# Optimization experiments

Measured on AMD Instinct MI355X. Metric: run time of the kernel, lower is better.

Reference implementation:

```python
import jax, jax.numpy as jnp
import numpy as np

STRIDE, PAD, DIL, DG, K = 1, 1, 1, 1, 3


def _conv2d(x, w, b, stride, pad):
    out = jax.lax.conv_general_dilated(
        x, w, (stride, stride), [(pad, pad), (pad, pad)],
        dimension_numbers=("NCHW", "OIHW", "NCHW"))
    return out + b[None, :, None, None]


def _deform_conv(x, weight, bias, offset, mask):
    # x: [B,C,H,W]; offset: [B, 2*DG*K*K, Ho, Wo] (y,x interleaved per tap);
    # mask: [B, DG*K*K, Ho, Wo]; weight: [Cout, C, K, K]
    B, C, H, W = x.shape
    Cout = weight.shape[0]
    KK = K * K
    Ho, Wo = offset.shape[2], offset.shape[3]
    Cg = C // DG

    off = offset.reshape(B, DG, KK, 2, Ho, Wo)
    dy, dx = off[:, :, :, 0], off[:, :, :, 1]          # [B,DG,KK,Ho,Wo]

    ky = (jnp.arange(KK) // K).astype(jnp.float32) * DIL
    kx = (jnp.arange(KK) % K).astype(jnp.float32) * DIL
    oy = (jnp.arange(Ho).astype(jnp.float32) * STRIDE - PAD)
    ox = (jnp.arange(Wo).astype(jnp.float32) * STRIDE - PAD)
    py = dy + ky[None, None, :, None, None] + oy[None, None, None, :, None]
    px = dx + kx[None, None, :, None, None] + ox[None, None, None, None, :]

    y0 = jnp.floor(py)
    x0 = jnp.floor(px)
    wy = py - y0
    wx = px - x0
    y0i = y0.astype(jnp.int32)
    x0i = x0.astype(jnp.int32)

    x_g = x.reshape(B, DG, Cg, H * W)
    val = jnp.zeros((B, DG, Cg, KK, Ho, Wo), dtype=x.dtype)
    corners = [(y0i, x0i, (1 - wy) * (1 - wx)),
               (y0i, x0i + 1, (1 - wy) * wx),
               (y0i + 1, x0i, wy * (1 - wx)),
               (y0i + 1, x0i + 1, wy * wx)]
    for iy, ix, wgt in corners:
        valid = ((iy >= 0) & (iy < H) & (ix >= 0) & (ix < W)).astype(x.dtype)
        idx = jnp.clip(iy, 0, H - 1) * W + jnp.clip(ix, 0, W - 1)  # [B,DG,KK,Ho,Wo]
        g = jnp.take_along_axis(x_g, idx.reshape(B, DG, 1, KK * Ho * Wo), axis=3)
        g = g.reshape(B, DG, Cg, KK, Ho, Wo)
        val = val + g * (wgt * valid)[:, :, None]

    m = mask.reshape(B, DG, 1, KK, Ho, Wo)
    val = (val * m).reshape(B, C, KK, Ho, Wo)
    out = jnp.einsum("bckhw,ock->bohw", val, weight.reshape(Cout, C, KK))
    return out + bias[None, :, None, None]


def setup_inputs() -> dict:
    key = jax.random.key(0)
    ks = jax.random.split(key, 5)
    B, C, H, W, Cout = 8, 64, 128, 128, 64
    x = jax.random.normal(ks[0], (B, C, H, W), dtype=jnp.float32)
    stdv = 1.0 / np.sqrt(C * K * K)
    weight = jax.random.uniform(ks[1], (Cout, C, K, K), minval=-stdv, maxval=stdv, dtype=jnp.float32)
    bias = jnp.zeros((Cout,), dtype=jnp.float32)
    # conv_offset params are zero-init in the original; use small random values
    offset_w = jax.random.normal(ks[2], (3 * DG * K * K, C, K, K), dtype=jnp.float32) * 0.01
    offset_b = jax.random.normal(ks[3], (3 * DG * K * K,), dtype=jnp.float32) * 0.01
    return {"x": x, "weight": weight, "bias": bias, "offset_w": offset_w, "offset_b": offset_b}


def reference(x, weight, bias, offset_w, offset_b):
    split = 2 * DG * K * K
    out = _conv2d(x, offset_w, offset_b, STRIDE, PAD)
    offset = out[:, :split]
    mask = jax.nn.sigmoid(out[:, split:])
    return _deform_conv(x, weight, bias, offset, mask)
```

## Files before the change

### kernel.cpp

```cpp
#include <hip/hip_runtime.h>
#include <hip/hip_bf16.h>
#include <math.h>

#define HH 128
#define WW 128
#define HW 16384
#define BATCH 8

#define TR 8
#define TC 16
#define HALO 2
#define PR 12
#define PC 20
#define NPX (PR * PC)
#define PST 34

typedef __attribute__((ext_vector_type(8))) _Float16 f16x8;
typedef __attribute__((ext_vector_type(2))) _Float16 f16x2;
typedef __attribute__((ext_vector_type(16))) float f32x16;
typedef __attribute__((ext_vector_type(4))) unsigned int u32x4;

union FragU { f16x8 v; unsigned int u[4]; u32x4 q; f16x2 h[4]; };

static __device__ __forceinline__ unsigned short f2h(float f) {
    _Float16 h = (_Float16)f;
    return *(unsigned short*)&h;
}
static __device__ __forceinline__ float h2f(unsigned short u) {
    _Float16 h = *(_Float16*)&u;
    return (float)h;
}

static __device__ __forceinline__ f16x8 bilerp_frag(
    u32x4 r00, u32x4 r01, u32x4 r10, u32x4 r11,
    f16x2 W0, f16x2 W1, f16x2 W2, f16x2 W3)
{
    FragU a, b, c, d, bf;
    a.q = r00; b.q = r01; c.q = r10; d.q = r11;
#pragma unroll
    for (int i = 0; i < 4; ++i) {
        f16x2 s = a.h[i] * W0;
        s = __builtin_elementwise_fma(b.h[i], W1, s);
        s = __builtin_elementwise_fma(c.h[i], W2, s);
        s = __builtin_elementwise_fma(d.h[i], W3, s);
        bf.h[i] = s;
    }
    return bf.v;
}

#define PADDR(PX, C) ((PX) * PST + ((C) << 2))

__global__ __launch_bounds__(256) void prep_kernel(
    const float* __restrict__ weight,
    const float* __restrict__ offset_w,
    unsigned short* __restrict__ wA,
    unsigned short* __restrict__ owA)
{
    int id = blockIdx.x * 256 + threadIdx.x;
    if (id < 4608) {
        int m = id / 2304;
        int rem = id % 2304;
        int kk = rem >> 8;
        int s = (rem >> 6) & 3;
        int l = id & 63;
        int cout = m * 32 + (l & 31);
        int cbase = s * 16 + 8 * (l >> 5);
#pragma unroll
        for (int j = 0; j < 8; ++j) {
            wA[id * 8 + j] = f2h(weight[(cout * 64 + cbase + j) * 9 + kk]);
        }
        return;
    }
    int id2 = id - 4608;
    if (id2 < 2304) {
        int kk = id2 >> 8;
        int s = (id2 >> 6) & 3;
        int l = id2 & 63;
        int cout = l & 31;
        int cbase = s * 16 + 8 * (l >> 5);
#pragma unroll
        for (int j = 0; j < 8; ++j) {
            float v = (cout < 27) ? offset_w[(cout * 64 + cbase + j) * 9 + kk] : 0.0f;
            owA[id2 * 8 + j] = f2h(v);
        }
    }
}

__global__ __launch_bounds__(256) void transform_kernel(
    const float* __restrict__ x,
    unsigned int* __restrict__ xT)
{
    __shared__ unsigned int lds[64][33];
    int bid = blockIdx.x;
    int b = bid & 7;
    int pix0 = (bid >> 3) << 6;
    int t = threadIdx.x;
    int px = t & 63;
    int cp0 = (t >> 6) * 8;

    const float* xb = x + (size_t)b * 64 * HW + pix0 + px;
#pragma unroll
    for (int it = 0; it < 8; ++it) {
        int cpair = cp0 + it;
        float lo = xb[(size_t)(2 * cpair) * HW];
        float hi = xb[(size_t)(2 * cpair + 1) * HW];
        lds[px][cpair] = ((unsigned int)f2h(hi) << 16) | f2h(lo);
    }
    __syncthreads();

    int wpx = t >> 2, qq = t & 3;
    unsigned int* dst = xT + ((size_t)b * HW + pix0 + wpx) * 32 + qq * 8;
    u32x4 a, c;
#pragma unroll
    for (int j = 0; j < 4; ++j) a[j] = lds[wpx][qq * 8 + j];
#pragma unroll
    for (int j = 0; j < 4; ++j) c[j] = lds[wpx][qq * 8 + 4 + j];
    *(u32x4*)dst = a;
    *(u32x4*)(dst + 4) = c;
}

__global__ __launch_bounds__(256, 4) void fused_kernel(
    const unsigned int* __restrict__ xT,
    const unsigned short* __restrict__ wA,
    const unsigned short* __restrict__ owA,
    const float* __restrict__ bias,
    const float* __restrict__ offset_b,
    float* __restrict__ out)
{
    __shared__ unsigned int patch[NPX * PST];
    __shared__ unsigned short red[4][27][32];

    int t = threadIdx.x;
    int lane = t & 63;
    int wid = t >> 6;
    int bid = blockIdx.x;
    int b = bid & 7;
    int tile = bid >> 3;
    int ho0 = (tile >> 3) * TR;
    int wo0 = (tile & 7) * TC;
    int py0 = ho0 - HALO;
    int px0 = wo0 - HALO;

    int q = lane & 31;
    int hi = lane >> 5;
    int ho = ho0 + 2 * wid + (q >> 4);
    int wo = wo0 + (q & 15);
    int p = ho * WW + wo;

    const unsigned int* xb = xT + (size_t)b * HW * 32;
    const f16x8* wAv = (const f16x8*)wA;
    const f16x8* owAv = (const f16x8*)owA;

#pragma unroll
    for (int it = 0; it < 8; ++it) {
        int id = it * 256 + t;
        if (id < NPX * 8) {
            int px = id >> 3;
            int c = id & 7;
            int row = px / PC;
            int col = px - row * PC;
            int iy = py0 + row;
            int ix = px0 + col;
            bool okpx = ((unsigned)iy < 128u) && ((unsigned)ix < 128u);
            int yc = min(max(iy, 0), HH - 1);
            int xc = min(max(ix, 0), WW - 1);
            u32x4 v = *(const u32x4*)(xb + (size_t)(yc * WW + xc) * 32 + c * 4);
#pragma unroll
            for (int j = 0; j < 4; ++j) v[j] = okpx ? v[j] : 0u;
            *(u32x4*)&patch[PADDR(px, c)] = v;
        }
    }
    __syncthreads();

    {
        f32x16 acc1 = {};
#pragma unroll
        for (int kk = 0; kk < 9; ++kk) {
            int jy = ho + kk / 3 - 1 - py0;
            int jx = wo + kk % 3 - 1 - px0;
            int ptap = jy * PC + jx;
#pragma unroll
            for (int s = 0; s < 4; ++s) {
                FragU bf;
                bf.q = *(const u32x4*)&patch[PADDR(ptap, 2 * s + hi)];
                acc1 = __builtin_amdgcn_mfma_f32_32x32x16_f16(
                    owAv[(kk * 4 + s) * 64 + lane], bf.v, acc1, 0, 0, 0);
            }
        }
#pragma unroll
        for (int r = 0; r < 16; ++r) {
            int cout = (r & 3) + 8 * (r >> 2) + 4 * hi;
            if (cout < 27) {
                float a = acc1[r] + offset_b[cout];
                if (cout >= 18) a = 1.0f / (1.0f + __expf(-a));
                red[wid][cout][q] = f2h(a);
            }
        }
    }

    f32x16 acc[2];
#pragma unroll
    for (int m = 0; m < 2; ++m) {
#pragma unroll
        for (int r = 0; r < 16; ++r) {
            acc[m][r] = bias[m * 32 + (r & 3) + 8 * (r >> 2) + 4 * hi];
        }
    }

    for (int kk = 0; kk < 9; ++kk) {
        float dy = h2f(red[wid][2 * kk][q]);
        float dx = h2f(red[wid][2 * kk + 1][q]);
        float mm = h2f(red[wid][18 + kk][q]);

        float py = dy + (float)(kk / 3 + ho - 1);
        float px = dx + (float)(kk % 3 + wo - 1);
        float y0f = floorf(py), x0f = floorf(px);
        float wy = py - y0f, wx = px - x0f;
        int y0 = (int)y0f, x0 = (int)x0f;
        int y1 = y0 + 1, x1 = x0 + 1;
        bool y0ok = (unsigned)y0 < 128u, y1ok = (unsigned)y1 < 128u;
        bool x0ok = (unsigned)x0 < 128u, x1ok = (unsigned)x1 < 128u;
        float w0 = (y0ok && x0ok) ? (1.0f - wy) * (1.0f - wx) * mm : 0.0f;
        float w1 = (y0ok && x1ok) ? (1.0f - wy) * wx * mm : 0.0f;
        float w2 = (y1ok && x0ok) ? wy * (1.0f - wx) * mm : 0.0f;
        float w3 = (y1ok && x1ok) ? wy * wx * mm : 0.0f;
        int y0c = min(max(y0, 0), 127), y1c = min(max(y1, 0), 127);
        int x0c = min(max(x0, 0), 127), x1c = min(max(x1, 0), 127);

        f16x2 W0 = {(_Float16)w0, (_Float16)w0};
        f16x2 W1 = {(_Float16)w1, (_Float16)w1};
        f16x2 W2 = {(_Float16)w2, (_Float16)w2};
        f16x2 W3 = {(_Float16)w3, (_Float16)w3};

        int jy0 = y0c - py0, jy1 = y1c - py0;
        int jx0 = x0c - px0, jx1 = x1c - px0;
        bool inp = ((unsigned)jy0 < (unsigned)PR) && ((unsigned)jy1 < (unsigned)PR) &&
                   ((unsigned)jx0 < (unsigned)PC) && ((unsigned)jx1 < (unsigned)PC);

#define P2_STEP(S, R00, R01, R10, R11) {                                    \
            f16x8 A0 = wAv[(kk * 4 + (S)) * 64 + lane];                     \
            f16x8 A1 = wAv[(36 + kk * 4 + (S)) * 64 + lane];                \
            f16x8 bf = bilerp_frag(R00, R01, R10, R11, W0, W1, W2, W3);     \
            acc[0] = __builtin_amdgcn_mfma_f32_32x32x16_f16(A0, bf, acc[0], 0, 0, 0); \
            acc[1] = __builtin_amdgcn_mfma_f32_32x32x16_f16(A1, bf, acc[1], 0, 0, 0); \
        }

        if (__all(inp)) {
            int p00 = jy0 * PC + jx0;
            int p01 = jy0 * PC + jx1;
            int p10 = jy1 * PC + jx0;
            int p11 = jy1 * PC + jx1;
#define LRD(PX, S) (*(const u32x4*)&patch[PADDR(PX, 2 * (S) + hi)])
            P2_STEP(0, LRD(p00,0), LRD(p01,0), LRD(p10,0), LRD(p11,0));
            P2_STEP(1, LRD(p00,1), LRD(p01,1), LRD(p10,1), LRD(p11,1));
            P2_STEP(2, LRD(p00,2), LRD(p01,2), LRD(p10,2), LRD(p11,2));
            P2_STEP(3, LRD(p00,3), LRD(p01,3), LRD(p10,3), LRD(p11,3));
#undef LRD
        } else {
            int o00 = (y0c * WW + x0c) * 32 + (hi << 2);
            int o01 = (y0c * WW + x1c) * 32 + (hi << 2);
            int o10 = (y1c * WW + x0c) * 32 + (hi << 2);
            int o11 = (y1c * WW + x1c) * 32 + (hi << 2);
#define GRD(O, S) (*(const u32x4*)(xb + (O) + (S) * 8))
            P2_STEP(0, GRD(o00,0), GRD(o01,0), GRD(o10,0), GRD(o11,0));
            P2_STEP(1, GRD(o00,1), GRD(o01,1), GRD(o10,1), GRD(o11,1));
            P2_STEP(2, GRD(o00,2), GRD(o01,2), GRD(o10,2), GRD(o11,2));
            P2_STEP(3, GRD(o00,3), GRD(o01,3), GRD(o10,3), GRD(o11,3));
#undef GRD
        }
#undef P2_STEP
    }

#pragma unroll
    for (int m = 0; m < 2; ++m) {
#pragma unroll
        for (int r = 0; r < 16; ++r) {
            int cout = m * 32 + (r & 3) + 8 * (r >> 2) + 4 * hi;
            out[((size_t)b * 64 + cout) * HW + p] = acc[m][r];
        }
    }
}

extern "C" void kernel_launch(void* const* d_in, const int* in_sizes, int n_in,
                              void* d_out, int out_size, void* d_ws, size_t ws_size,
                              hipStream_t stream) {
    const float* x        = (const float*)d_in[0];
    const float* weight   = (const float*)d_in[1];
    const float* bias     = (const float*)d_in[2];
    const float* offset_w = (const float*)d_in[3];
    const float* offset_b = (const float*)d_in[4];
    float* out = (float*)d_out;

    unsigned int* xT = (unsigned int*)d_ws;
    unsigned short* wA  = (unsigned short*)(xT + (size_t)BATCH * HW * 32);
    unsigned short* owA = wA + 4608 * 8;

    prep_kernel<<<27, 256, 0, stream>>>(weight, offset_w, wA, owA);

    int n_tiles = BATCH * HW / 64;
    transform_kernel<<<n_tiles, 256, 0, stream>>>(x, xT);

    int n_blocks = BATCH * HW / 128;
    fused_kernel<<<n_blocks, 256, 0, stream>>>(xT, wA, owA, bias, offset_b, out);
}
```

Measured before the change: 52.80 us.

## Merge prep and transform kernels; software-pipeline bilinear gather loads in fused kernel

The weight-prep and NCHW-to-channel-last transform kernels are merged into one launch, with the weight work placed in 27 extra blocks, so one kernel launch and its gap go away. In the main deformable loop, the per-tap sampling context is computed into a struct, and the four corner loads for the next channel slice (or the next tap) are issued before the current slice's bilinear blend and MFMAs. This double-buffers the LDS and global gathers to hide their latency behind the matrix math. The cost is more live registers, which could hurt occupancy under the 4-waves launch bound or cause spills.

```diff
diff --git a/kernel.cpp b/kernel.cpp
--- a/kernel.cpp
+++ b/kernel.cpp
@@ -50,13 +50,54 @@
 
 #define PADDR(PX, C) ((PX) * PST + ((C) << 2))
 
-__global__ __launch_bounds__(256) void prep_kernel(
+struct Ctx {
+    f16x2 W0, W1, W2, W3;
+    int p00, p01, p10, p11;
+    int g00, g01, g10, g11;
+    int inp;
+};
+
+__global__ __launch_bounds__(256) void transform_prep_kernel(
+    const float* __restrict__ x,
+    unsigned int* __restrict__ xT,
     const float* __restrict__ weight,
     const float* __restrict__ offset_w,
     unsigned short* __restrict__ wA,
     unsigned short* __restrict__ owA)
 {
-    int id = blockIdx.x * 256 + threadIdx.x;
+    __shared__ unsigned int lds[64][33];
+    int bid = blockIdx.x;
+    int t = threadIdx.x;
+
+    if (bid < 2048) {
+        int b = bid & 7;
+        int pix0 = (bid >> 3) << 6;
+        int px = t & 63;
+        int cp0 = (t >> 6) * 8;
+
+        const float* xb = x + (size_t)b * 64 * HW + pix0 + px;
+#pragma unroll
+        for (int it = 0; it < 8; ++it) {
+            int cpair = cp0 + it;
+            float lo = xb[(size_t)(2 * cpair) * HW];
+            float hi = xb[(size_t)(2 * cpair + 1) * HW];
+            lds[px][cpair] = ((unsigned int)f2h(hi) << 16) | f2h(lo);
+        }
+        __syncthreads();
+
+        int wpx = t >> 2, qq = t & 3;
+        unsigned int* dst = xT + ((size_t)b * HW + pix0 + wpx) * 32 + qq * 8;
+        u32x4 a, c;
+#pragma unroll
+        for (int j = 0; j < 4; ++j) a[j] = lds[wpx][qq * 8 + j];
+#pragma unroll
+        for (int j = 0; j < 4; ++j) c[j] = lds[wpx][qq * 8 + 4 + j];
+        *(u32x4*)dst = a;
+        *(u32x4*)(dst + 4) = c;
+        return;
+    }
+
+    int id = (bid - 2048) * 256 + t;
     if (id < 4608) {
         int m = id / 2304;
         int rem = id % 2304;
@@ -84,39 +125,6 @@
             owA[id2 * 8 + j] = f2h(v);
         }
     }
-}
-
-__global__ __launch_bounds__(256) void transform_kernel(
-    const float* __restrict__ x,
-    unsigned int* __restrict__ xT)
-{
-    __shared__ unsigned int lds[64][33];
-    int bid = blockIdx.x;
-    int b = bid & 7;
-    int pix0 = (bid >> 3) << 6;
-    int t = threadIdx.x;
-    int px = t & 63;
-    int cp0 = (t >> 6) * 8;
-
-    const float* xb = x + (size_t)b * 64 * HW + pix0 + px;
-#pragma unroll
-    for (int it = 0; it < 8; ++it) {
-        int cpair = cp0 + it;
-        float lo = xb[(size_t)(2 * cpair) * HW];
-        float hi = xb[(size_t)(2 * cpair + 1) * HW];
-        lds[px][cpair] = ((unsigned int)f2h(hi) << 16) | f2h(lo);
-    }
-    __syncthreads();
-
-    int wpx = t >> 2, qq = t & 3;
-    unsigned int* dst = xT + ((size_t)b * HW + pix0 + wpx) * 32 + qq * 8;
-    u32x4 a, c;
-#pragma unroll
-    for (int j = 0; j < 4; ++j) a[j] = lds[wpx][qq * 8 + j];
-#pragma unroll
-    for (int j = 0; j < 4; ++j) c[j] = lds[wpx][qq * 8 + 4 + j];
-    *(u32x4*)dst = a;
-    *(u32x4*)(dst + 4) = c;
 }
 
 __global__ __launch_bounds__(256, 4) void fused_kernel(
@@ -207,69 +215,93 @@
         }
     }
 
-    for (int kk = 0; kk < 9; ++kk) {
-        float dy = h2f(red[wid][2 * kk][q]);
-        float dx = h2f(red[wid][2 * kk + 1][q]);
-        float mm = h2f(red[wid][18 + kk][q]);
-
-        float py = dy + (float)(kk / 3 + ho - 1);
-        float px = dx + (float)(kk % 3 + wo - 1);
-        float y0f = floorf(py), x0f = floorf(px);
-        float wy = py - y0f, wx = px - x0f;
-        int y0 = (int)y0f, x0 = (int)x0f;
-        int y1 = y0 + 1, x1 = x0 + 1;
-        bool y0ok = (unsigned)y0 < 128u, y1ok = (unsigned)y1 < 128u;
-        bool x0ok = (unsigned)x0 < 128u, x1ok = (unsigned)x1 < 128u;
-        float w0 = (y0ok && x0ok) ? (1.0f - wy) * (1.0f - wx) * mm : 0.0f;
-        float w1 = (y0ok && x1ok) ? (1.0f - wy) * wx * mm : 0.0f;
-        float w2 = (y1ok && x0ok) ? wy * (1.0f - wx) * mm : 0.0f;
-        float w3 = (y1ok && x1ok) ? wy * wx * mm : 0.0f;
-        int y0c = min(max(y0, 0), 127), y1c = min(max(y1, 0), 127);
-        int x0c = min(max(x0, 0), 127), x1c = min(max(x1, 0), 127);
-
-        f16x2 W0 = {(_Float16)w0, (_Float16)w0};
-        f16x2 W1 = {(_Float16)w1, (_Float16)w1};
-        f16x2 W2 = {(_Float16)w2, (_Float16)w2};
-        f16x2 W3 = {(_Float16)w3, (_Float16)w3};
-
-        int jy0 = y0c - py0, jy1 = y1c - py0;
-        int jx0 = x0c - px0, jx1 = x1c - px0;
-        bool inp = ((unsigned)jy0 < (unsigned)PR) && ((unsigned)jy1 < (unsigned)PR) &&
-                   ((unsigned)jx0 < (unsigned)PC) && ((unsigned)jx1 < (unsigned)PC);
-
-#define P2_STEP(S, R00, R01, R10, R11) {                                    \
-            f16x8 A0 = wAv[(kk * 4 + (S)) * 64 + lane];                     \
-            f16x8 A1 = wAv[(36 + kk * 4 + (S)) * 64 + lane];                \
-            f16x8 bf = bilerp_frag(R00, R01, R10, R11, W0, W1, W2, W3);     \
-            acc[0] = __builtin_amdgcn_mfma_f32_32x32x16_f16(A0, bf, acc[0], 0, 0, 0); \
-            acc[1] = __builtin_amdgcn_mfma_f32_32x32x16_f16(A1, bf, acc[1], 0, 0, 0); \
-        }
-
-        if (__all(inp)) {
-            int p00 = jy0 * PC + jx0;
-            int p01 = jy0 * PC + jx1;
-            int p10 = jy1 * PC + jx0;
-            int p11 = jy1 * PC + jx1;
-#define LRD(PX, S) (*(const u32x4*)&patch[PADDR(PX, 2 * (S) + hi)])
-            P2_STEP(0, LRD(p00,0), LRD(p01,0), LRD(p10,0), LRD(p11,0));
-            P2_STEP(1, LRD(p00,1), LRD(p01,1), LRD(p10,1), LRD(p11,1));
-            P2_STEP(2, LRD(p00,2), LRD(p01,2), LRD(p10,2), LRD(p11,2));
-            P2_STEP(3, LRD(p00,3), LRD(p01,3), LRD(p10,3), LRD(p11,3));
-#undef LRD
-        } else {
-            int o00 = (y0c * WW + x0c) * 32 + (hi << 2);
-            int o01 = (y0c * WW + x1c) * 32 + (hi << 2);
-            int o10 = (y1c * WW + x0c) * 32 + (hi << 2);
-            int o11 = (y1c * WW + x1c) * 32 + (hi << 2);
-#define GRD(O, S) (*(const u32x4*)(xb + (O) + (S) * 8))
-            P2_STEP(0, GRD(o00,0), GRD(o01,0), GRD(o10,0), GRD(o11,0));
-            P2_STEP(1, GRD(o00,1), GRD(o01,1), GRD(o10,1), GRD(o11,1));
-            P2_STEP(2, GRD(o00,2), GRD(o01,2), GRD(o10,2), GRD(o11,2));
-            P2_STEP(3, GRD(o00,3), GRD(o01,3), GRD(o10,3), GRD(o11,3));
-#undef GRD
-        }
-#undef P2_STEP
-    }
+#define MKCTX(KK, KY, KX, C) {                                              \
+        float dy = h2f(red[wid][2 * (KK)][q]);                              \
+        float dx = h2f(red[wid][2 * (KK) + 1][q]);                          \
+        float mm = h2f(red[wid][18 + (KK)][q]);                             \
+        float py_ = dy + (float)((KY) + ho - 1);                            \
+        float px_ = dx + (float)((KX) + wo - 1);                            \
+        float y0f = floorf(py_), x0f = floorf(px_);                         \
+        float wy = py_ - y0f, wx = px_ - x0f;                               \
+        int y0 = (int)y0f, x0 = (int)x0f;                                   \
+        int y1 = y0 + 1, x1 = x0 + 1;                                       \
+        bool y0ok = (unsigned)y0 < 128u, y1ok = (unsigned)y1 < 128u;        \
+        bool x0ok = (unsigned)x0 < 128u, x1ok = (unsigned)x1 < 128u;        \
+        float w0 = (y0ok && x0ok) ? (1.0f - wy) * (1.0f - wx) * mm : 0.0f;  \
+        float w1 = (y0ok && x1ok) ? (1.0f - wy) * wx * mm : 0.0f;           \
+        float w2 = (y1ok && x0ok) ? wy * (1.0f - wx) * mm : 0.0f;           \
+        float w3 = (y1ok && x1ok) ? wy * wx * mm : 0.0f;                    \
+        C.W0 = (f16x2){(_Float16)w0, (_Float16)w0};                         \
+        C.W1 = (f16x2){(_Float16)w1, (_Float16)w1};                         \
+        C.W2 = (f16x2){(_Float16)w2, (_Float16)w2};                         \
+        C.W3 = (f16x2){(_Float16)w3, (_Float16)w3};                         \
+        int y0c = min(max(y0, 0), 127), y1c = min(max(y1, 0), 127);         \
+        int x0c = min(max(x0, 0), 127), x1c = min(max(x1, 0), 127);         \
+        int jy0 = y0c - py0, jy1 = y1c - py0;                               \
+        int jx0 = x0c - px0, jx1 = x1c - px0;                               \
+        bool inp_ = ((unsigned)jy0 < (unsigned)PR) &&                       \
+                    ((unsigned)jy1 < (unsigned)PR) &&                       \
+                    ((unsigned)jx0 < (unsigned)PC) &&                       \
+                    ((unsigned)jx1 < (unsigned)PC);                         \
+        C.inp = __all(inp_);                                                \
+        C.p00 = jy0 * PC + jx0; C.p01 = jy0 * PC + jx1;                     \
+        C.p10 = jy1 * PC + jx0; C.p11 = jy1 * PC + jx1;                     \
+        C.g00 = (y0c * WW + x0c) * 32 + (hi << 2);                          \
+        C.g01 = (y0c * WW + x1c) * 32 + (hi << 2);                          \
+        C.g10 = (y1c * WW + x0c) * 32 + (hi << 2);                          \
+        C.g11 = (y1c * WW + x1c) * 32 + (hi << 2);                          \
+    }
+
+#define LDC(C, S, R00, R01, R10, R11) {                                     \
+        if (C.inp) {                                                        \
+            R00 = *(const u32x4*)&patch[PADDR(C.p00, 2 * (S) + hi)];        \
+            R01 = *(const u32x4*)&patch[PADDR(C.p01, 2 * (S) + hi)];        \
+            R10 = *(const u32x4*)&patch[PADDR(C.p10, 2 * (S) + hi)];        \
+            R11 = *(const u32x4*)&patch[PADDR(C.p11, 2 * (S) + hi)];        \
+        } else {                                                            \
+            R00 = *(const u32x4*)(xb + C.g00 + (S) * 8);                    \
+            R01 = *(const u32x4*)(xb + C.g01 + (S) * 8);                    \
+            R10 = *(const u32x4*)(xb + C.g10 + (S) * 8);                    \
+            R11 = *(const u32x4*)(xb + C.g11 + (S) * 8);                    \
+        }                                                                   \
+    }
+
+#define DO_STEP(KK, S, C, R00, R01, R10, R11) {                             \
+        f16x8 A0 = wAv[((KK) * 4 + (S)) * 64 + lane];                       \
+        f16x8 A1 = wAv[(36 + (KK) * 4 + (S)) * 64 + lane];                  \
+        f16x8 bf = bilerp_frag(R00, R01, R10, R11, C.W0, C.W1, C.W2, C.W3); \
+        acc[0] = __builtin_amdgcn_mfma_f32_32x32x16_f16(A0, bf, acc[0], 0, 0, 0); \
+        acc[1] = __builtin_amdgcn_mfma_f32_32x32x16_f16(A1, bf, acc[1], 0, 0, 0); \
+    }
+
+    {
+        Ctx cc;
+        MKCTX(0, 0, 0, cc);
+        u32x4 r00, r01, r10, r11, n00, n01, n10, n11;
+        LDC(cc, 0, r00, r01, r10, r11);
+
+        int ky = 0, kx = 0;
+        for (int kk = 0; kk < 9; ++kk) {
+            LDC(cc, 1, n00, n01, n10, n11);
+            DO_STEP(kk, 0, cc, r00, r01, r10, r11);
+            r00 = n00; r01 = n01; r10 = n10; r11 = n11;
+            LDC(cc, 2, n00, n01, n10, n11);
+            DO_STEP(kk, 1, cc, r00, r01, r10, r11);
+            r00 = n00; r01 = n01; r10 = n10; r11 = n11;
+            LDC(cc, 3, n00, n01, n10, n11);
+            DO_STEP(kk, 2, cc, r00, r01, r10, r11);
+            r00 = n00; r01 = n01; r10 = n10; r11 = n11;
+            DO_STEP(kk, 3, cc, r00, r01, r10, r11);
+            if (kk < 8) {
+                kx++; if (kx == 3) { kx = 0; ky++; }
+                MKCTX(kk + 1, ky, kx, cc);
+                LDC(cc, 0, r00, r01, r10, r11);
+            }
+        }
+    }
+#undef MKCTX
+#undef LDC
+#undef DO_STEP
 
 #pragma unroll
     for (int m = 0; m < 2; ++m) {
@@ -295,10 +327,8 @@
     unsigned short* wA  = (unsigned short*)(xT + (size_t)BATCH * HW * 32);
     unsigned short* owA = wA + 4608 * 8;
 
-    prep_kernel<<<27, 256, 0, stream>>>(weight, offset_w, wA, owA);
-
-    int n_tiles = BATCH * HW / 64;
-    transform_kernel<<<n_tiles, 256, 0, stream>>>(x, xT);
+    int n_tp = BATCH * HW / 64 + 27;
+    transform_prep_kernel<<<n_tp, 256, 0, stream>>>(x, xT, weight, offset_w, wA, owA);
 
     int n_blocks = BATCH * HW / 128;
     fused_kernel<<<n_blocks, 256, 0, stream>>>(xT, wA, owA, bias, offset_b, out);
```

Measured after the change: 80.51 us. 52.5% more time.
